# Kernel tuning notes

Hardware: AMD Instinct MI355X
Metric: run time of the kernel (lower is better)

The kernel has to match this reference:

```python
import jax, jax.numpy as jnp
import numpy as np

H = 8        # heads
DH = 64      # dim_head
IMG = 32     # image_size
KS = 5       # kernel_size (odd)
SCALE = DH ** -0.5


def _unfold(t, ks):
    # t: (b, c, Hp, Wp) already padded. Returns (b, c*ks*ks, Ho*Wo) with
    # channel-major layout (c outermost, then kh, kw) matching torch F.unfold.
    b, c, Hp, Wp = t.shape
    Ho, Wo = Hp - ks + 1, Wp - ks + 1
    pat = jnp.stack([t[:, :, i:i + Ho, j:j + Wo]
                     for i in range(ks) for j in range(ks)], axis=2)  # (b,c,ks*ks,Ho,Wo)
    return pat.reshape(b, c * ks * ks, Ho * Wo)


def setup_inputs() -> dict:
    key = jax.random.key(0)
    k1, k2, k3, k4 = jax.random.split(key, 4)
    b, n, dim, inner = 2, 1152, 512, 512
    x = jax.random.normal(k1, (b, n, dim), jnp.float32)
    w_qkv = jax.random.normal(k2, (dim, inner * 3), jnp.float32) * 0.02
    w_out = jax.random.normal(k3, (inner, dim), jnp.float32) * 0.02
    b_out = jax.random.normal(k4, (dim,), jnp.float32) * 0.02
    return {"x": x, "w_qkv": w_qkv, "w_out": w_out, "b_out": b_out}


def reference(x, w_qkv, w_out, b_out):
    b, n, dim = x.shape
    img_len = IMG * IMG
    text_len = n - img_len
    NEG = -jnp.finfo(x.dtype).max

    qkv = x @ w_qkv                                   # (b, n, 3*inner)
    q, k, v = jnp.split(qkv, 3, axis=-1)

    def to_heads(t):
        return t.reshape(b, n, H, DH).transpose(0, 2, 1, 3).reshape(b * H, n, DH)

    q = to_heads(q) * SCALE
    k = to_heads(k)
    v = to_heads(v)

    # faithful to source: text slice is t[:, img_seq_len:], image is t[:, -img_seq_len:]
    q_text, q_img = q[:, img_len:], q[:, -img_len:]
    k_text, k_img = k[:, img_len:], k[:, -img_len:]
    v_text, v_img = v[:, img_len:], v[:, -img_len:]

    # ---- text branch. NOTE: source uses non-inplace masked_fill, so the
    # causal mask has NO effect -> plain softmax (faithful reproduction).
    dots_text = jnp.einsum('bid,bjd->bij', q_text, k_text)
    attn_text = jax.nn.softmax(dots_text, axis=-1)
    out_text = jnp.einsum('bij,bjd->bid', attn_text, v_text)

    # ---- image branch: local window via unfold
    def to_loc(t):
        g = t.transpose(0, 2, 1).reshape(b * H, DH, IMG, IMG)
        p = KS // 2
        g = jnp.pad(g, ((0, 0), (0, 0), (p, p), (p, p)))
        u = _unfold(g, KS)  # (bh, DH*KS*KS, img_len), channel-major (d outer)
        # faithful to source rearrange 'b (j d) i -> b i j d' (j outermost),
        # which regroups the channel-major unfold output.
        return u.reshape(b * H, KS * KS, DH, img_len).transpose(0, 3, 1, 2)

    k_loc = to_loc(k_img)  # (bh, img_len, KS*KS, DH)
    v_loc = to_loc(v_img)

    dots_txt = jnp.einsum('bid,bjd->bij', q_img, k_text)     # (bh, img_len, text_len)
    dots_loc = jnp.einsum('bid,bijd->bij', q_img, k_loc)     # (bh, img_len, KS*KS)

    # per-query key index mask (padded positions get index img_len -> never masked)
    p = KS // 2
    idx = jnp.arange(img_len, dtype=jnp.float32).reshape(1, 1, IMG, IMG)
    idx = jnp.pad(idx, ((0, 0), (0, 0), (p, p), (p, p)), constant_values=float(img_len))
    kidx = _unfold(idx, KS).transpose(0, 2, 1)               # (1, img_len, KS*KS)
    qidx = jnp.arange(img_len, dtype=jnp.float32).reshape(1, -1, 1)
    mask_loc = qidx <= kidx                                  # faithful: keep q <= k
    dots_loc = jnp.where(mask_loc, dots_loc, NEG)

    dots_img = jnp.concatenate([dots_txt, dots_loc], axis=-1)
    attn_img = jax.nn.softmax(dots_img, axis=-1)
    out_img = (jnp.einsum('bij,bjd->bid', attn_img[..., :text_len], v_text)
               + jnp.einsum('bij,bijd->bid', attn_img[..., text_len:], v_loc))

    out = jnp.concatenate([out_text, out_img], axis=1)       # (bh, n, DH)
    out = out.reshape(b, H, n, DH).transpose(0, 2, 1, 3).reshape(b, n, H * DH)
    return out @ w_out + b_out
```

## Files before the change

### kernel.cpp

```cpp
#include <hip/hip_runtime.h>
#include <hip/hip_bf16.h>
#include <math.h>

#define NTOK 1152
#define DIM 512
#define NQKV 1536
#define DHEAD 64
#define NBH 16
#define TEXTN 128
#define IMGLEN 1024
#define SEG (NBH * NTOK * DHEAD)
#define STF 68
#define TSTATE_F (NBH * IMGLEN * STF)
#define LPAD 40
#define KTSZ (NBH * TEXTN * DHEAD)

typedef __attribute__((ext_vector_type(8))) short bf16x8;
typedef __attribute__((ext_vector_type(4))) float f32x4;

__device__ __forceinline__ ushort f2bf(float f) {
    unsigned u = __float_as_uint(f);
    unsigned r = (u + 0x7FFFu + ((u >> 16) & 1u)) >> 16;
    return (ushort)r;
}
__device__ __forceinline__ float bf2f(ushort u) {
    return __uint_as_float(((unsigned)u) << 16);
}

__global__ __launch_bounds__(256) void prep_x_k(const float* __restrict__ X,
                                                ushort* __restrict__ xhi,
                                                ushort* __restrict__ xlo) {
    int i = (blockIdx.x * 256 + threadIdx.x) * 4;
    float4 v = *(const float4*)(X + i);
    ushort4 h, l;
    h.x = f2bf(v.x); l.x = f2bf(v.x - bf2f(h.x));
    h.y = f2bf(v.y); l.y = f2bf(v.y - bf2f(h.y));
    h.z = f2bf(v.z); l.z = f2bf(v.z - bf2f(h.z));
    h.w = f2bf(v.w); l.w = f2bf(v.w - bf2f(h.w));
    *(ushort4*)(xhi + i) = h;
    *(ushort4*)(xlo + i) = l;
}

__global__ __launch_bounds__(256) void prep_wt_k(const float* __restrict__ W,
                                                 ushort* __restrict__ thi,
                                                 ushort* __restrict__ tlo,
                                                 int K, int N) {
    __shared__ float tile[32][33];
    const int bx = blockIdx.x, by = blockIdx.y;
    const int c = threadIdx.x & 31, r8 = threadIdx.x >> 5;
#pragma unroll
    for (int i = 0; i < 4; ++i) {
        int rr = r8 + i * 8;
        tile[rr][c] = W[(size_t)(by * 32 + rr) * N + bx * 32 + c];
    }
    __syncthreads();
#pragma unroll
    for (int i = 0; i < 4; ++i) {
        int rr = r8 + i * 8;
        float v = tile[c][rr];
        size_t o = (size_t)(bx * 32 + rr) * K + by * 32 + c;
        ushort h = f2bf(v);
        thi[o] = h;
        tlo[o] = f2bf(v - bf2f(h));
    }
}

__global__ __launch_bounds__(256) void gemm_qkv_mfma(const ushort* __restrict__ xhi,
                                                     const ushort* __restrict__ xlo,
                                                     const ushort* __restrict__ wthi,
                                                     const ushort* __restrict__ wtlo,
                                                     float* __restrict__ qh,
                                                     float* __restrict__ kh,
                                                     float* __restrict__ vh,
                                                     ushort* __restrict__ qhi,
                                                     ushort* __restrict__ qlo,
                                                     ushort* __restrict__ kthi,
                                                     ushort* __restrict__ ktlo,
                                                     ushort* __restrict__ vthi,
                                                     ushort* __restrict__ vtlo) {
    __shared__ __align__(16) ushort Ah[128 * LPAD], Al[128 * LPAD];
    __shared__ __align__(16) ushort Bh[64 * LPAD], Bl[64 * LPAD];
    const int tid = threadIdx.x;
    const int lane = tid & 63;
    const int w = tid >> 6;
    const int wm = w >> 1, wn = w & 1;
    const int row0 = blockIdx.y * 128;
    const int col0 = blockIdx.x * 64;

    f32x4 acc[4][2];
#pragma unroll
    for (int a = 0; a < 4; ++a)
#pragma unroll
        for (int b = 0; b < 2; ++b) acc[a][b] = (f32x4){0.f, 0.f, 0.f, 0.f};

    const int arow = tid >> 1;
    const int akb = (tid & 1) * 16;
    const int brow = tid >> 2;
    const int bkb = (tid & 3) * 8;
    const int kf = (lane >> 4) * 8;
    const int lr = lane & 15;

    for (int k0 = 0; k0 < DIM; k0 += 32) {
        {
            const size_t g = (size_t)(row0 + arow) * DIM + k0 + akb;
            *(bf16x8*)&Ah[arow * LPAD + akb] = *(const bf16x8*)(xhi + g);
            *(bf16x8*)&Ah[arow * LPAD + akb + 8] = *(const bf16x8*)(xhi + g + 8);
            *(bf16x8*)&Al[arow * LPAD + akb] = *(const bf16x8*)(xlo + g);
            *(bf16x8*)&Al[arow * LPAD + akb + 8] = *(const bf16x8*)(xlo + g + 8);
        }
        {
            const size_t g = (size_t)(col0 + brow) * DIM + k0 + bkb;
            *(bf16x8*)&Bh[brow * LPAD + bkb] = *(const bf16x8*)(wthi + g);
            *(bf16x8*)&Bl[brow * LPAD + bkb] = *(const bf16x8*)(wtlo + g);
        }
        __syncthreads();
        bf16x8 ah[4], al[4], bh[2], bl[2];
#pragma unroll
        for (int mi = 0; mi < 4; ++mi) {
            int rr = wm * 64 + mi * 16 + lr;
            ah[mi] = *(const bf16x8*)&Ah[rr * LPAD + kf];
            al[mi] = *(const bf16x8*)&Al[rr * LPAD + kf];
        }
#pragma unroll
        for (int ni = 0; ni < 2; ++ni) {
            int rr = wn * 32 + ni * 16 + lr;
            bh[ni] = *(const bf16x8*)&Bh[rr * LPAD + kf];
            bl[ni] = *(const bf16x8*)&Bl[rr * LPAD + kf];
        }
#pragma unroll
        for (int mi = 0; mi < 4; ++mi)
#pragma unroll
            for (int ni = 0; ni < 2; ++ni) {
                acc[mi][ni] = __builtin_amdgcn_mfma_f32_16x16x32_bf16(ah[mi], bh[ni], acc[mi][ni], 0, 0, 0);
                acc[mi][ni] = __builtin_amdgcn_mfma_f32_16x16x32_bf16(ah[mi], bl[ni], acc[mi][ni], 0, 0, 0);
                acc[mi][ni] = __builtin_amdgcn_mfma_f32_16x16x32_bf16(al[mi], bh[ni], acc[mi][ni], 0, 0, 0);
            }
        __syncthreads();
    }

    const int which = col0 >> 9;
    const int hh = (col0 & 511) >> 6;
    const float scale = (which == 0) ? 0.125f : 1.f;
    float* dst = (which == 0) ? qh : ((which == 1) ? kh : vh);
#pragma unroll
    for (int mi = 0; mi < 4; ++mi)
#pragma unroll
        for (int ni = 0; ni < 2; ++ni)
#pragma unroll
            for (int j = 0; j < 4; ++j) {
                int r = row0 + wm * 64 + mi * 16 + (lane >> 4) * 4 + j;
                int b_i = r / NTOK, tok = r - b_i * NTOK;
                int d = wn * 32 + ni * 16 + (lane & 15);
                int bhi = b_i * 8 + hh;
                float val = acc[mi][ni][j] * scale;
                dst[((size_t)bhi * NTOK + tok) * DHEAD + d] = val;
                if (which == 0) {
                    size_t qo = ((size_t)bhi * NTOK + tok) * DHEAD + d;
                    ushort h2 = f2bf(val);
                    qhi[qo] = h2;
                    qlo[qo] = f2bf(val - bf2f(h2));
                } else if (tok >= IMGLEN) {
                    int tr = tok - IMGLEN;
                    ushort h2 = f2bf(val);
                    ushort l2 = f2bf(val - bf2f(h2));
                    if (which == 1) {
                        size_t ko = ((size_t)bhi * TEXTN + tr) * DHEAD + d;
                        kthi[ko] = h2; ktlo[ko] = l2;
                    } else {
                        size_t vo = ((size_t)bhi * DHEAD + d) * TEXTN + tr;
                        vthi[vo] = h2; vtlo[vo] = l2;
                    }
                }
            }
}

__global__ __launch_bounds__(256) void attn_text_mfma(const ushort* __restrict__ qhi,
                                                      const ushort* __restrict__ qlo,
                                                      const ushort* __restrict__ kthi,
                                                      const ushort* __restrict__ ktlo,
                                                      const ushort* __restrict__ vthi,
                                                      const ushort* __restrict__ vtlo,
                                                      ushort* __restrict__ ahi,
                                                      ushort* __restrict__ alo,
                                                      float* __restrict__ tstate) {
    __shared__ __align__(16) ushort Phi[4][16][136];
    __shared__ __align__(16) ushort Plo[4][16][136];
    const int bh = blockIdx.x / 18;
    const int tile = blockIdx.x % 18;
    const int wave = threadIdx.x >> 6;
    const int lane = threadIdx.x & 63;
    const int lr = lane & 15, lg = lane >> 4;
    const int kf = lg * 8;
    const int qrow0 = tile * 64 + wave * 16;
    const int tok0 = (tile < 2 ? 1024 + tile * 64 : tile * 64) + wave * 16;

    bf16x8 qah[2], qal[2];
    {
        const size_t qb = ((size_t)bh * NTOK + tok0 + lr) * DHEAD;
#pragma unroll
        for (int c = 0; c < 2; ++c) {
            qah[c] = *(const bf16x8*)(qhi + qb + c * 32 + kf);
            qal[c] = *(const bf16x8*)(qlo + qb + c * 32 + kf);
        }
    }
    f32x4 s[8];
#pragma unroll
    for (int t = 0; t < 8; ++t) s[t] = (f32x4){0.f, 0.f, 0.f, 0.f};
#pragma unroll
    for (int t = 0; t < 8; ++t) {
        const size_t kb = ((size_t)bh * TEXTN + t * 16 + lr) * DHEAD;
#pragma unroll
        for (int c = 0; c < 2; ++c) {
            bf16x8 kbh = *(const bf16x8*)(kthi + kb + c * 32 + kf);
            bf16x8 kbl = *(const bf16x8*)(ktlo + kb + c * 32 + kf);
            s[t] = __builtin_amdgcn_mfma_f32_16x16x32_bf16(qah[c], kbh, s[t], 0, 0, 0);
            s[t] = __builtin_amdgcn_mfma_f32_16x16x32_bf16(qah[c], kbl, s[t], 0, 0, 0);
            s[t] = __builtin_amdgcn_mfma_f32_16x16x32_bf16(qal[c], kbh, s[t], 0, 0, 0);
        }
    }
    float mx[4], sm[4];
#pragma unroll
    for (int r = 0; r < 4; ++r) {
        float v = s[0][r];
#pragma unroll
        for (int t = 1; t < 8; ++t) v = fmaxf(v, s[t][r]);
        mx[r] = v;
    }
#pragma unroll
    for (int msk = 1; msk <= 8; msk <<= 1)
#pragma unroll
        for (int r = 0; r < 4; ++r) mx[r] = fmaxf(mx[r], __shfl_xor(mx[r], msk));
#pragma unroll
    for (int r = 0; r < 4; ++r) sm[r] = 0.f;
#pragma unroll
    for (int t = 0; t < 8; ++t)
#pragma unroll
        for (int r = 0; r < 4; ++r) {
            float p = __expf(s[t][r] - mx[r]);
            s[t][r] = p;
            sm[r] += p;
        }
#pragma unroll
    for (int msk = 1; msk <= 8; msk <<= 1)
#pragma unroll
        for (int r = 0; r < 4; ++r) sm[r] += __shfl_xor(sm[r], msk);
#pragma unroll
    for (int t = 0; t < 8; ++t)
#pragma unroll
        for (int r = 0; r < 4; ++r) {
            float p = s[t][r];
            ushort h = f2bf(p);
            Phi[wave][lg * 4 + r][t * 16 + lr] = h;
            Plo[wave][lg * 4 + r][t * 16 + lr] = f2bf(p - bf2f(h));
        }
    __syncthreads();
    f32x4 o[4];
#pragma unroll
    for (int dt = 0; dt < 4; ++dt) o[dt] = (f32x4){0.f, 0.f, 0.f, 0.f};
#pragma unroll
    for (int c = 0; c < 4; ++c) {
        bf16x8 pah = *(const bf16x8*)&Phi[wave][lr][c * 32 + kf];
        bf16x8 pal = *(const bf16x8*)&Plo[wave][lr][c * 32 + kf];
#pragma unroll
        for (int dt = 0; dt < 4; ++dt) {
            const size_t vb = ((size_t)bh * DHEAD + dt * 16 + lr) * TEXTN + c * 32 + kf;
            bf16x8 vbh = *(const bf16x8*)(vthi + vb);
            bf16x8 vbl = *(const bf16x8*)(vtlo + vb);
            o[dt] = __builtin_amdgcn_mfma_f32_16x16x32_bf16(pah, vbh, o[dt], 0, 0, 0);
            o[dt] = __builtin_amdgcn_mfma_f32_16x16x32_bf16(pah, vbl, o[dt], 0, 0, 0);
            o[dt] = __builtin_amdgcn_mfma_f32_16x16x32_bf16(pal, vbh, o[dt], 0, 0, 0);
        }
    }
    if (tile < 2) {
#pragma unroll
        for (int r = 0; r < 4; ++r) {
            const int row = qrow0 + lg * 4 + r;
            const float inv = 1.f / sm[r];
            const size_t base = ((size_t)bh * NTOK + row) * DHEAD;
#pragma unroll
            for (int dt = 0; dt < 4; ++dt) {
                float v = o[dt][r] * inv;
                ushort h = f2bf(v);
                ahi[base + dt * 16 + lr] = h;
                alo[base + dt * 16 + lr] = f2bf(v - bf2f(h));
            }
        }
    } else {
#pragma unroll
        for (int r = 0; r < 4; ++r) {
            const int imgq = qrow0 - TEXTN + lg * 4 + r;
            float* st = tstate + ((size_t)bh * IMGLEN + imgq) * STF;
#pragma unroll
            for (int dt = 0; dt < 4; ++dt) st[dt * 16 + lr] = o[dt][r];
            if (lr == 0) { st[64] = mx[r]; st[65] = sm[r]; }
        }
    }
}

template <int W>
__device__ inline void loc_dots(const float* __restrict__ kimg, int y, int x,
                                const float (&q)[64], float (&sd)[25]) {
#pragma unroll
    for (int t = 0; t < 25; ++t) {
        const int ny = y + t / 5 - 2;
        const int nx = x + t % 5 - 2;
        if (ny >= 0 && ny < 32 && nx >= 0 && nx < 32) {
            const float* kp = kimg + (size_t)(ny * 32 + nx) * DHEAD + W * 16;
#pragma unroll
            for (int g = 0; g < 4; ++g) {
                float4 kv = *(const float4*)(kp + g * 4);
                float ke[4] = {kv.x, kv.y, kv.z, kv.w};
#pragma unroll
                for (int e = 0; e < 4; ++e) {
                    const int d = W * 16 + g * 4 + e;
                    const int id2 = d * 25 + t;
                    sd[id2 >> 6] += q[id2 & 63] * ke[e];
                }
            }
        }
    }
}

template <int W>
__device__ inline void loc_pv(const float* __restrict__ vimg, int y, int x,
                              const float (&p)[25], float (&po)[64]) {
#pragma unroll
    for (int t = 0; t < 25; ++t) {
        const int ny = y + t / 5 - 2;
        const int nx = x + t % 5 - 2;
        if (ny >= 0 && ny < 32 && nx >= 0 && nx < 32) {
            const float* vp = vimg + (size_t)(ny * 32 + nx) * DHEAD + W * 16;
#pragma unroll
            for (int g = 0; g < 4; ++g) {
                float4 vv = *(const float4*)(vp + g * 4);
                float ve[4] = {vv.x, vv.y, vv.z, vv.w};
#pragma unroll
                for (int e = 0; e < 4; ++e) {
                    const int d = W * 16 + g * 4 + e;
                    const int id2 = d * 25 + t;
                    po[id2 & 63] += p[id2 >> 6] * ve[e];
                }
            }
        }
    }
}

__global__ __launch_bounds__(256) void attn_img_k(const float* __restrict__ qh,
                                                  const float* __restrict__ kh,
                                                  const float* __restrict__ vh,
                                                  ushort* __restrict__ ahi,
                                                  ushort* __restrict__ alo,
                                                  const float* __restrict__ tstate) {
    __shared__ float sdb[4][64][27];
    __shared__ float pob[2][64][68];
    const int bh = blockIdx.x >> 4;
    const int qtile = (blockIdx.x & 15) << 6;
    const int wave = threadIdx.x >> 6;
    const int lane = threadIdx.x & 63;
    const int qq = qtile + lane;
    const int y = qq >> 5, x = qq & 31;
    const float* kimg = kh + (size_t)(bh * NTOK + TEXTN) * DHEAD;
    const float* vimg = vh + (size_t)(bh * NTOK + TEXTN) * DHEAD;
    const float* st = tstate + ((size_t)(bh * IMGLEN + qq)) * STF;

    float sd[25];
#pragma unroll
    for (int j = 0; j < 25; ++j) sd[j] = 0.f;
    {
        float q[64];
        const float* qp = qh + ((size_t)(bh * NTOK + TEXTN + qq)) * DHEAD;
#pragma unroll
        for (int g = 0; g < 16; ++g) {
            float4 v4 = *(const float4*)(qp + g * 4);
            q[g * 4] = v4.x; q[g * 4 + 1] = v4.y; q[g * 4 + 2] = v4.z; q[g * 4 + 3] = v4.w;
        }
        if (wave == 0) loc_dots<0>(kimg, y, x, q, sd);
        else if (wave == 1) loc_dots<1>(kimg, y, x, q, sd);
        else if (wave == 2) loc_dots<2>(kimg, y, x, q, sd);
        else loc_dots<3>(kimg, y, x, q, sd);
    }
#pragma unroll
    for (int j = 0; j < 25; ++j) sdb[wave][lane][j] = sd[j];
    __syncthreads();

    float p[25];
#pragma unroll
    for (int j = 0; j < 25; ++j)
        p[j] = (sdb[0][lane][j] + sdb[1][lane][j]) + (sdb[2][lane][j] + sdb[3][lane][j]);
    float m = st[64], l = st[65];
    float mloc = -1e30f;
#pragma unroll
    for (int j = 0; j < 25; ++j) {
        const int my = y + j / 5 - 2;
        const int mx = x + j % 5 - 2;
        bool inb = (my >= 0 && my < 32 && mx >= 0 && mx < 32);
        bool keep = inb ? (qq <= my * 32 + mx) : true;
        p[j] = keep ? p[j] : -1e30f;
        mloc = fmaxf(mloc, p[j]);
    }
    const float M = fmaxf(m, mloc);
    const float cc = __expf(m - M);
    l *= cc;
#pragma unroll
    for (int j = 0; j < 25; ++j) {
        p[j] = __expf(p[j] - M);
        l += p[j];
    }
    const float inv = 1.f / l;

    float po[64];
#pragma unroll
    for (int o = 0; o < 64; ++o) po[o] = 0.f;
    if (wave == 0) loc_pv<0>(vimg, y, x, p, po);
    else if (wave == 1) loc_pv<1>(vimg, y, x, p, po);
    else if (wave == 2) loc_pv<2>(vimg, y, x, p, po);
    else loc_pv<3>(vimg, y, x, p, po);

    if (wave < 2) {
#pragma unroll
        for (int o = 0; o < 64; ++o) pob[wave][lane][o] = po[o];
    }
    __syncthreads();
    if (wave >= 2) {
#pragma unroll
        for (int o = 0; o < 64; ++o) pob[wave - 2][lane][o] += po[o];
    }
    __syncthreads();

    {
        const float* stq = st + wave * 16;
        size_t base = ((size_t)(bh * NTOK + TEXTN + qq)) * DHEAD + wave * 16;
#pragma unroll
        for (int g = 0; g < 4; ++g) {
            float4 tv = *(const float4*)(stq + g * 4);
            float4 a0 = *(const float4*)&pob[0][lane][wave * 16 + g * 4];
            float4 a1 = *(const float4*)&pob[1][lane][wave * 16 + g * 4];
            float v0 = (a0.x + a1.x + cc * tv.x) * inv;
            float v1 = (a0.y + a1.y + cc * tv.y) * inv;
            float v2 = (a0.z + a1.z + cc * tv.z) * inv;
            float v3 = (a0.w + a1.w + cc * tv.w) * inv;
            ushort4 oh, ol;
            oh.x = f2bf(v0); ol.x = f2bf(v0 - bf2f(oh.x));
            oh.y = f2bf(v1); ol.y = f2bf(v1 - bf2f(oh.y));
            oh.z = f2bf(v2); ol.z = f2bf(v2 - bf2f(oh.z));
            oh.w = f2bf(v3); ol.w = f2bf(v3 - bf2f(oh.w));
            *(ushort4*)(ahi + base + g * 4) = oh;
            *(ushort4*)(alo + base + g * 4) = ol;
        }
    }
}

__global__ __launch_bounds__(256) void gemm_out_mfma(const ushort* __restrict__ ahi,
                                                     const ushort* __restrict__ alo,
                                                     const ushort* __restrict__ wthi,
                                                     const ushort* __restrict__ wtlo,
                                                     const float* __restrict__ bias,
                                                     float* __restrict__ Y) {
    __shared__ __align__(16) ushort Ah[128 * LPAD], Al[128 * LPAD];
    __shared__ __align__(16) ushort Bh[64 * LPAD], Bl[64 * LPAD];
    const int tid = threadIdx.x;
    const int lane = tid & 63;
    const int w = tid >> 6;
    const int wm = w >> 1, wn = w & 1;
    const int row0 = blockIdx.y * 128;
    const int col0 = blockIdx.x * 64;

    f32x4 acc[4][2];
#pragma unroll
    for (int a = 0; a < 4; ++a)
#pragma unroll
        for (int b = 0; b < 2; ++b) acc[a][b] = (f32x4){0.f, 0.f, 0.f, 0.f};

    const int arow = tid >> 1;
    const int akb = (tid & 1) * 16;
    const int brow = tid >> 2;
    const int bkb = (tid & 3) * 8;
    const int kf = (lane >> 4) * 8;
    const int lr = lane & 15;

    const int ar = row0 + arow;
    const int a_bi = ar / NTOK;
    const int a_tok = ar - a_bi * NTOK;

    for (int k0 = 0; k0 < DIM; k0 += 32) {
        {
            const int kg = k0 + akb;
            const int hh = kg >> 6, d0 = kg & 63;
            const size_t g = ((size_t)(a_bi * 8 + hh) * NTOK + a_tok) * DHEAD + d0;
            *(bf16x8*)&Ah[arow * LPAD + akb] = *(const bf16x8*)(ahi + g);
            *(bf16x8*)&Ah[arow * LPAD + akb + 8] = *(const bf16x8*)(ahi + g + 8);
            *(bf16x8*)&Al[arow * LPAD + akb] = *(const bf16x8*)(alo + g);
            *(bf16x8*)&Al[arow * LPAD + akb + 8] = *(const bf16x8*)(alo + g + 8);
        }
        {
            const size_t g = (size_t)(col0 + brow) * DIM + k0 + bkb;
            *(bf16x8*)&Bh[brow * LPAD + bkb] = *(const bf16x8*)(wthi + g);
            *(bf16x8*)&Bl[brow * LPAD + bkb] = *(const bf16x8*)(wtlo + g);
        }
        __syncthreads();
        bf16x8 ah[4], al[4], bh[2], bl[2];
#pragma unroll
        for (int mi = 0; mi < 4; ++mi) {
            int rr = wm * 64 + mi * 16 + lr;
            ah[mi] = *(const bf16x8*)&Ah[rr * LPAD + kf];
            al[mi] = *(const bf16x8*)&Al[rr * LPAD + kf];
        }
#pragma unroll
        for (int ni = 0; ni < 2; ++ni) {
            int rr = wn * 32 + ni * 16 + lr;
            bh[ni] = *(const bf16x8*)&Bh[rr * LPAD + kf];
            bl[ni] = *(const bf16x8*)&Bl[rr * LPAD + kf];
        }
#pragma unroll
        for (int mi = 0; mi < 4; ++mi)
#pragma unroll
            for (int ni = 0; ni < 2; ++ni) {
                acc[mi][ni] = __builtin_amdgcn_mfma_f32_16x16x32_bf16(ah[mi], bh[ni], acc[mi][ni], 0, 0, 0);
                acc[mi][ni] = __builtin_amdgcn_mfma_f32_16x16x32_bf16(ah[mi], bl[ni], acc[mi][ni], 0, 0, 0);
                acc[mi][ni] = __builtin_amdgcn_mfma_f32_16x16x32_bf16(al[mi], bh[ni], acc[mi][ni], 0, 0, 0);
            }
        __syncthreads();
    }

#pragma unroll
    for (int mi = 0; mi < 4; ++mi)
#pragma unroll
        for (int ni = 0; ni < 2; ++ni) {
            int cidx = col0 + wn * 32 + ni * 16 + (lane & 15);
            float bv = bias[cidx];
#pragma unroll
            for (int j = 0; j < 4; ++j) {
                int r = row0 + wm * 64 + mi * 16 + (lane >> 4) * 4 + j;
                Y[(size_t)r * DIM + cidx] = acc[mi][ni][j] + bv;
            }
        }
}

extern "C" void kernel_launch(void* const* d_in, const int* in_sizes, int n_in,
                              void* d_out, int out_size, void* d_ws, size_t ws_size,
                              hipStream_t stream) {
    const float* x = (const float*)d_in[0];
    const float* w_qkv = (const float*)d_in[1];
    const float* w_out = (const float*)d_in[2];
    const float* b_out = (const float*)d_in[3];
    float* Y = (float*)d_out;
    float* ws = (float*)d_ws;
    float* qh = ws;
    float* kh = ws + (size_t)SEG;
    float* vh = ws + 2 * (size_t)SEG;
    float* tstate = ws + 3 * (size_t)SEG;
    ushort* xhi = (ushort*)(ws + 3 * (size_t)SEG + TSTATE_F);
    ushort* xlo = xhi + (size_t)SEG;
    ushort* ahi = xhi;
    ushort* alo = xlo;
    ushort* wqthi = xlo + (size_t)SEG;
    ushort* wqtlo = wqthi + (size_t)DIM * NQKV;
    ushort* wothi = wqtlo + (size_t)DIM * NQKV;
    ushort* wotlo = wothi + (size_t)DIM * DIM;
    ushort* qhi = wotlo + (size_t)DIM * DIM;
    ushort* qlo = qhi + (size_t)SEG;
    ushort* kthi = qlo + (size_t)SEG;
    ushort* ktlo = kthi + (size_t)KTSZ;
    ushort* vthi = ktlo + (size_t)KTSZ;
    ushort* vtlo = vthi + (size_t)KTSZ;

    hipLaunchKernelGGL(prep_x_k, dim3(SEG / 1024), dim3(256), 0, stream, x, xhi, xlo);
    hipLaunchKernelGGL(prep_wt_k, dim3(NQKV / 32, DIM / 32), dim3(256), 0, stream,
                       w_qkv, wqthi, wqtlo, DIM, NQKV);
    hipLaunchKernelGGL(prep_wt_k, dim3(DIM / 32, DIM / 32), dim3(256), 0, stream,
                       w_out, wothi, wotlo, DIM, DIM);
    hipLaunchKernelGGL(gemm_qkv_mfma, dim3(NQKV / 64, 2304 / 128), dim3(256), 0, stream,
                       xhi, xlo, wqthi, wqtlo, qh, kh, vh,
                       qhi, qlo, kthi, ktlo, vthi, vtlo);
    hipLaunchKernelGGL(attn_text_mfma, dim3(NBH * 18), dim3(256), 0, stream,
                       qhi, qlo, kthi, ktlo, vthi, vtlo, ahi, alo, tstate);
    hipLaunchKernelGGL(attn_img_k, dim3(NBH * 16), dim3(256), 0, stream,
                       qh, kh, vh, ahi, alo, tstate);
    hipLaunchKernelGGL(gemm_out_mfma, dim3(DIM / 64, 2304 / 128), dim3(256), 0, stream,
                       ahi, alo, wothi, wotlo, b_out, Y);
}
```

Before: 132.3 us.

## Split image local-attention block across eight waves instead of four

The image-branch local attention kernel now runs 512 threads per block. Each wave computes the dot products for 8 head dimensions instead of 16, and the P·V work is split so each wave covers 16 dims over half of the 25 window taps. Partial results are reduced through one aliased shared buffer with extra barriers. The goal is more parallelism and latency hiding in a grid of only 256 blocks, at the cost of more synchronisation and shared-memory reduction traffic.

```diff
diff --git a/kernel.cpp b/kernel.cpp
--- a/kernel.cpp
+++ b/kernel.cpp
@@ -297,35 +297,33 @@
     }
 }
 
-template <int W>
-__device__ inline void loc_dots(const float* __restrict__ kimg, int y, int x,
-                                const float (&q)[64], float (&sd)[25]) {
+template <int W8>
+__device__ inline void loc_dots8(const float* __restrict__ kimg, int y, int x,
+                                 const float (&q)[64], float (&sd)[25]) {
 #pragma unroll
     for (int t = 0; t < 25; ++t) {
         const int ny = y + t / 5 - 2;
         const int nx = x + t % 5 - 2;
         if (ny >= 0 && ny < 32 && nx >= 0 && nx < 32) {
-            const float* kp = kimg + (size_t)(ny * 32 + nx) * DHEAD + W * 16;
-#pragma unroll
-            for (int g = 0; g < 4; ++g) {
-                float4 kv = *(const float4*)(kp + g * 4);
-                float ke[4] = {kv.x, kv.y, kv.z, kv.w};
-#pragma unroll
-                for (int e = 0; e < 4; ++e) {
-                    const int d = W * 16 + g * 4 + e;
-                    const int id2 = d * 25 + t;
-                    sd[id2 >> 6] += q[id2 & 63] * ke[e];
-                }
+            const float* kp = kimg + (size_t)(ny * 32 + nx) * DHEAD + W8 * 8;
+            float4 k0 = *(const float4*)kp;
+            float4 k1 = *(const float4*)(kp + 4);
+            float ke[8] = {k0.x, k0.y, k0.z, k0.w, k1.x, k1.y, k1.z, k1.w};
+#pragma unroll
+            for (int e = 0; e < 8; ++e) {
+                const int d = W8 * 8 + e;
+                const int id2 = d * 25 + t;
+                sd[id2 >> 6] += q[id2 & 63] * ke[e];
             }
         }
     }
 }
 
-template <int W>
-__device__ inline void loc_pv(const float* __restrict__ vimg, int y, int x,
-                              const float (&p)[25], float (&po)[64]) {
-#pragma unroll
-    for (int t = 0; t < 25; ++t) {
+template <int W, int T0, int T1>
+__device__ inline void loc_pvr(const float* __restrict__ vimg, int y, int x,
+                               const float (&p)[25], float (&po)[64]) {
+#pragma unroll
+    for (int t = T0; t < T1; ++t) {
         const int ny = y + t / 5 - 2;
         const int nx = x + t % 5 - 2;
         if (ny >= 0 && ny < 32 && nx >= 0 && nx < 32) {
@@ -345,14 +343,15 @@
     }
 }
 
-__global__ __launch_bounds__(256) void attn_img_k(const float* __restrict__ qh,
+__global__ __launch_bounds__(512) void attn_img_k(const float* __restrict__ qh,
                                                   const float* __restrict__ kh,
                                                   const float* __restrict__ vh,
                                                   ushort* __restrict__ ahi,
                                                   ushort* __restrict__ alo,
                                                   const float* __restrict__ tstate) {
-    __shared__ float sdb[4][64][27];
-    __shared__ float pob[2][64][68];
+    __shared__ __align__(16) float smem[8 * 64 * 26];
+    float (*sdb)[64][26] = reinterpret_cast<float (*)[64][26]>(smem);
+    float (*pob)[64][68] = reinterpret_cast<float (*)[64][68]>(smem);
     const int bh = blockIdx.x >> 4;
     const int qtile = (blockIdx.x & 15) << 6;
     const int wave = threadIdx.x >> 6;
@@ -374,10 +373,16 @@
             float4 v4 = *(const float4*)(qp + g * 4);
             q[g * 4] = v4.x; q[g * 4 + 1] = v4.y; q[g * 4 + 2] = v4.z; q[g * 4 + 3] = v4.w;
         }
-        if (wave == 0) loc_dots<0>(kimg, y, x, q, sd);
-        else if (wave == 1) loc_dots<1>(kimg, y, x, q, sd);
-        else if (wave == 2) loc_dots<2>(kimg, y, x, q, sd);
-        else loc_dots<3>(kimg, y, x, q, sd);
+        switch (wave) {
+            case 0: loc_dots8<0>(kimg, y, x, q, sd); break;
+            case 1: loc_dots8<1>(kimg, y, x, q, sd); break;
+            case 2: loc_dots8<2>(kimg, y, x, q, sd); break;
+            case 3: loc_dots8<3>(kimg, y, x, q, sd); break;
+            case 4: loc_dots8<4>(kimg, y, x, q, sd); break;
+            case 5: loc_dots8<5>(kimg, y, x, q, sd); break;
+            case 6: loc_dots8<6>(kimg, y, x, q, sd); break;
+            default: loc_dots8<7>(kimg, y, x, q, sd); break;
+        }
     }
 #pragma unroll
     for (int j = 0; j < 25; ++j) sdb[wave][lane][j] = sd[j];
@@ -386,7 +391,8 @@
     float p[25];
 #pragma unroll
     for (int j = 0; j < 25; ++j)
-        p[j] = (sdb[0][lane][j] + sdb[1][lane][j]) + (sdb[2][lane][j] + sdb[3][lane][j]);
+        p[j] = ((sdb[0][lane][j] + sdb[1][lane][j]) + (sdb[2][lane][j] + sdb[3][lane][j])) +
+               ((sdb[4][lane][j] + sdb[5][lane][j]) + (sdb[6][lane][j] + sdb[7][lane][j]));
     float m = st[64], l = st[65];
     float mloc = -1e30f;
 #pragma unroll
@@ -411,23 +417,40 @@
     float po[64];
 #pragma unroll
     for (int o = 0; o < 64; ++o) po[o] = 0.f;
-    if (wave == 0) loc_pv<0>(vimg, y, x, p, po);
-    else if (wave == 1) loc_pv<1>(vimg, y, x, p, po);
-    else if (wave == 2) loc_pv<2>(vimg, y, x, p, po);
-    else loc_pv<3>(vimg, y, x, p, po);
+    switch (wave) {
+        case 0: loc_pvr<0, 0, 13>(vimg, y, x, p, po); break;
+        case 1: loc_pvr<1, 0, 13>(vimg, y, x, p, po); break;
+        case 2: loc_pvr<2, 0, 13>(vimg, y, x, p, po); break;
+        case 3: loc_pvr<3, 0, 13>(vimg, y, x, p, po); break;
+        case 4: loc_pvr<0, 13, 25>(vimg, y, x, p, po); break;
+        case 5: loc_pvr<1, 13, 25>(vimg, y, x, p, po); break;
+        case 6: loc_pvr<2, 13, 25>(vimg, y, x, p, po); break;
+        default: loc_pvr<3, 13, 25>(vimg, y, x, p, po); break;
+    }
+    __syncthreads();
 
     if (wave < 2) {
 #pragma unroll
         for (int o = 0; o < 64; ++o) pob[wave][lane][o] = po[o];
     }
     __syncthreads();
-    if (wave >= 2) {
+    if (wave >= 2 && wave < 4) {
 #pragma unroll
         for (int o = 0; o < 64; ++o) pob[wave - 2][lane][o] += po[o];
     }
     __syncthreads();
-
-    {
+    if (wave >= 4 && wave < 6) {
+#pragma unroll
+        for (int o = 0; o < 64; ++o) pob[wave - 4][lane][o] += po[o];
+    }
+    __syncthreads();
+    if (wave >= 6) {
+#pragma unroll
+        for (int o = 0; o < 64; ++o) pob[wave - 6][lane][o] += po[o];
+    }
+    __syncthreads();
+
+    if (wave < 4) {
         const float* stq = st + wave * 16;
         size_t base = ((size_t)(bh * NTOK + TEXTN + qq)) * DHEAD + wave * 16;
 #pragma unroll
@@ -574,7 +597,7 @@
                        qhi, qlo, kthi, ktlo, vthi, vtlo);
     hipLaunchKernelGGL(attn_text_mfma, dim3(NBH * 18), dim3(256), 0, stream,
                        qhi, qlo, kthi, ktlo, vthi, vtlo, ahi, alo, tstate);
-    hipLaunchKernelGGL(attn_img_k, dim3(NBH * 16), dim3(256), 0, stream,
+    hipLaunchKernelGGL(attn_img_k, dim3(NBH * 16), dim3(512), 0, stream,
                        qh, kh, vh, ahi, alo, tstate);
     hipLaunchKernelGGL(gemm_out_mfma, dim3(DIM / 64, 2304 / 128), dim3(256), 0, stream,
                        ahi, alo, wothi, wotlo, b_out, Y);
```

After: 133.6 us. About the same (+1.0%).
